# Kernel tuning notes

Hardware: AMD Instinct MI355X
Metric: run time of the kernel (lower is better)

The kernel has to match this reference:

```python
import jax, jax.numpy as jnp
import numpy as np

# dims: batch N, channels C, fine nodes V, coarse nodes VC, super nodes S, time L
N, C, V, VC, S, L, CO = 16, 32, 2048, 256, 64, 12, 32
N1, N2, N3, N4 = 0.8, 0.2, 0.2, 0.2  # residual fusion scales


def asym_adj(a):
    # D^-1 A row-normalization (sp.diags(d_inv) @ A), inf -> 0
    rowsum = jnp.sum(a, axis=1)
    d_inv = jnp.where(rowsum > 0, 1.0 / rowsum, 0.0)
    return a * d_inv[:, None]


def nconv(x, a):
    return jnp.einsum('ncvl,vw->ncwl', x, a)


def gcn(x, supports, W, b):
    h = jnp.concatenate([x, nconv(x, supports[0]), nconv(x, supports[1])], axis=1)
    return jnp.einsum('nkvl,ok->novl', h, W) + b[None, :, None, None]


def hgcn_forward(x, support, support_c, acs, afc, W, b):
    hf = gcn(x, support, W, b)                               # fine level  [N,CO,V,L]
    xc = jnp.einsum('vw,ncvl->ncwl', afc, x)                 # afc.T @ x   [N,C,VC,L]
    hc = gcn(xc, support_c, W, b)                            # coarse level [N,CO,VC,L]
    sxg = jnp.einsum('ws,ncwl->ncsl', acs, xc)               # acs.T @ afc.T @ x [N,C,S,L]
    # faithful reproduction of torch permute/reshape (mismatched flatten orders)
    hs_flat = jnp.transpose(sxg, (2, 1, 0, 3)).reshape(S, -1)  # [S, C*N*L]
    hst = jnp.transpose(sxg, (3, 0, 1, 2)).reshape(-1, S)      # [L*N*C, S]
    as_mat = jax.lax.stop_gradient(jax.nn.relu(hs_flat @ hst - 0.5))  # detached [S,S]
    sup_s = [jax.nn.softmax(asym_adj(as_mat), axis=-1),
             jax.nn.softmax(asym_adj(as_mat.T), axis=-1)]
    hs = gcn(sxg, sup_s, W, b)                               # super level [N,CO,S,L]
    # hierarchical relu-scaled residual fusions
    hc = hc + N1 * jax.nn.relu(jnp.einsum('ws,ncsl->ncwl', acs, hs))
    hf = hf + N2 * jax.nn.relu(jnp.einsum('vw,ncwl->ncvl', afc, hc))
    hc = hc + N3 * jax.nn.relu(jnp.einsum('vw,ncvl->ncwl', afc, hf))
    hs = hs + N4 * jax.nn.relu(jnp.einsum('ws,ncwl->ncsl', acs, hc))
    return hf, hc, hs


def setup_inputs() -> dict:
    key = jax.random.key(0)
    k = jax.random.split(key, 7)
    x = jax.random.normal(k[0], (N, C, V, L), jnp.float32)
    support = jax.nn.softmax(jax.random.normal(k[1], (2, V, V), jnp.float32), axis=-1)
    support_c = jax.nn.softmax(jax.random.normal(k[2], (2, VC, VC), jnp.float32), axis=-1)
    acs = jax.random.normal(k[3], (VC, S), jnp.float32) * 0.05
    afc = jax.random.normal(k[4], (V, VC), jnp.float32) * 0.02
    W = jax.random.normal(k[5], (CO, 3 * C), jnp.float32) * 0.05  # 1x1 conv weight
    b = jax.random.normal(k[6], (CO,), jnp.float32) * 0.01
    return {"x": x, "support": support, "support_c": support_c, "acs": acs,
            "afc": afc, "W": W, "b": b}


def reference(x, support, support_c, acs, afc, W, b):
    return hgcn_forward(x, support, support_c, acs, afc, W, b)
```

## Files before the change

kernel.cpp:

```cpp
#include <hip/hip_runtime.h>

constexpr int NB = 16;
constexpr int CC = 32;
constexpr int VV = 2048;
constexpr int VCC = 256;
constexpr int SS = 64;
constexpr int LL = 12;
constexpr int CO = 32;
constexpr long MM = (long)NB * CO * LL;

typedef __attribute__((ext_vector_type(8))) __bf16 bf16x8;
typedef __attribute__((ext_vector_type(4))) float f32x4;

__device__ __forceinline__ unsigned short f2bf(float f) {
    unsigned u = __float_as_uint(f);
    unsigned r = u + 0x7FFFu + ((u >> 16) & 1u);
    return (unsigned short)(r >> 16);
}

__device__ __forceinline__ void gl_lds16(const void* g, void* l) {
    __builtin_amdgcn_global_load_lds(
        (const __attribute__((address_space(1))) void*)g,
        (__attribute__((address_space(3))) void*)l, 16, 0, 0);
}

__global__ __launch_bounds__(256)
void transpose_vl(const float* __restrict__ in, float* __restrict__ out,
                  unsigned short* __restrict__ outb) {
    __shared__ float t[128 * 12];
    const long nc = blockIdx.y;
    const int v0 = blockIdx.x * 128;
    const float* src = in + (nc * VV + v0) * 12;
    for (int f = threadIdx.x; f < 128 * 12; f += 256) t[f] = src[f];
    __syncthreads();
    float* dst = out + nc * 12L * VV;
    unsigned short* dstb = outb + nc * 12L * VV;
    for (int g = threadIdx.x; g < 128 * 12; g += 256) {
        int l = g >> 7, vv = g & 127;
        const float v = t[vv * 12 + l];
        dst[(long)l * VV + v0 + vv] = v;
        dstb[(long)l * VV + v0 + vv] = f2bf(v);
    }
}

__global__ __launch_bounds__(256)
void transpose_lv(const float* __restrict__ in, float* __restrict__ out, int Kn, int TW) {
    __shared__ float t[128 * 12];
    const long nc = blockIdx.y;
    const int v0 = blockIdx.x * TW;
    const float* src = in + nc * 12L * Kn;
    for (int g = threadIdx.x; g < TW * 12; g += 256) {
        int l = g / TW, vv = g - l * TW;
        t[vv * 12 + l] = src[(long)l * Kn + v0 + vv];
    }
    __syncthreads();
    float* dst = out + (nc * Kn + v0) * 12L;
    for (int f = threadIdx.x; f < TW * 12; f += 256) dst[f] = t[f];
}

__global__ __launch_bounds__(256)
void transpose2d(const float* __restrict__ in, float* __restrict__ out, int rows, int cols) {
    __shared__ float t[32][33];
    const int r0 = blockIdx.y * 32, c0 = blockIdx.x * 32;
    const int ty = threadIdx.x / 32, tx = threadIdx.x % 32;
    for (int i = ty; i < 32; i += 8) t[i][tx] = in[(long)(r0 + i) * cols + c0 + tx];
    __syncthreads();
    for (int i = ty; i < 32; i += 8) out[(long)(c0 + i) * rows + r0 + tx] = t[tx][i];
}

__global__ __launch_bounds__(256)
void cvt_bf16_k(const float* __restrict__ in, unsigned short* __restrict__ out, long n) {
    long i = ((long)blockIdx.x * 256 + threadIdx.x) * 4;
    if (i >= n) return;
    const float4 v = *(const float4*)(in + i);
    ushort4 o;
    o.x = f2bf(v.x); o.y = f2bf(v.y); o.z = f2bf(v.z); o.w = f2bf(v.w);
    *(ushort4*)(out + i) = o;
}

__global__ __launch_bounds__(256)
void cvt_T_bf16_k(const float* __restrict__ in, unsigned short* __restrict__ out,
                  int R, int Ccols) {
    __shared__ float t[32][33];
    const int r0 = blockIdx.y * 32, c0 = blockIdx.x * 32;
    const int ty = threadIdx.x / 32, tx = threadIdx.x % 32;
    for (int i = ty; i < 32; i += 8) t[i][tx] = in[(long)(r0 + i) * Ccols + c0 + tx];
    __syncthreads();
    for (int i = ty; i < 32; i += 8) out[(long)(c0 + i) * R + r0 + tx] = f2bf(t[tx][i]);
}

__global__ __launch_bounds__(256)
void chanmix_fine(const float* __restrict__ in, const float* __restrict__ Wt,
                  float* __restrict__ y0, unsigned short* __restrict__ y12) {
    __shared__ float Ws[CO * 96];
    for (int idx = threadIdx.x; idx < CO * 96; idx += 256) Ws[idx] = Wt[idx];
    __syncthreads();
    const int nb = blockIdx.y;
    const int r = blockIdx.x * 256 + threadIdx.x;
    const int R = LL * VV;
    const int l = r / VV, k = r - l * VV;
    float xv[CC];
#pragma unroll
    for (int c = 0; c < CC; ++c) xv[c] = in[((long)(nb * CC + c)) * R + r];
    for (int o = 0; o < CO; ++o) {
        float a0 = 0.f, a1 = 0.f, a2 = 0.f;
#pragma unroll
        for (int c = 0; c < CC; ++c) {
            const float x = xv[c];
            a0 = fmaf(Ws[o * 96 + c], x, a0);
            a1 = fmaf(Ws[o * 96 + 32 + c], x, a1);
            a2 = fmaf(Ws[o * 96 + 64 + c], x, a2);
        }
        const long mrow = (long)(nb * CO + o) * LL + l;
        y0[mrow * VV + k] = a0;
        y12[mrow * 4096 + k] = f2bf(a1);
        y12[mrow * 4096 + 2048 + k] = f2bf(a2);
    }
}

__global__ __launch_bounds__(256)
void chanmix_k(const float* __restrict__ in, const float* __restrict__ Wt,
               int R, int Kn, float* __restrict__ o0,
               float* __restrict__ o1, int ld1) {
    __shared__ float Ws[CO * 96];
    for (int idx = threadIdx.x; idx < CO * 96; idx += 256) Ws[idx] = Wt[idx];
    __syncthreads();
    const int nb = blockIdx.y;
    const int r = blockIdx.x * 256 + threadIdx.x;
    if (r >= R) return;
    const int l = r / Kn, k = r - l * Kn;
    float xv[CC];
#pragma unroll
    for (int c = 0; c < CC; ++c) xv[c] = in[((long)(nb * CC + c)) * R + r];
    for (int o = 0; o < CO; ++o) {
        float a0 = 0.f, a1 = 0.f, a2 = 0.f;
#pragma unroll
        for (int c = 0; c < CC; ++c) {
            const float x = xv[c];
            a0 = fmaf(Ws[o * 96 + c], x, a0);
            a1 = fmaf(Ws[o * 96 + 32 + c], x, a1);
            a2 = fmaf(Ws[o * 96 + 64 + c], x, a2);
        }
        const long mrow = (long)(nb * CO + o) * LL + l;
        o0[mrow * Kn + k] = a0;
        o1[mrow * ld1 + k] = a1;
        o1[mrow * ld1 + Kn + k] = a2;
    }
}

template <bool RELU, bool ADDC0, bool BIAS>
__global__ __launch_bounds__(256)
void gemm_mfma(const unsigned short* __restrict__ A, int lda,
               const unsigned short* __restrict__ Bt, int ldb,
               const float* __restrict__ C0, int ldc,
               const float* __restrict__ bias,
               float* __restrict__ Out, int ldo, int K, float alpha) {
    __shared__ __align__(16) unsigned short As[128 * 64];
    __shared__ __align__(16) unsigned short Bs[128 * 64];
    const int tid = threadIdx.x;
    const int lane = tid & 63;
    const int w = tid >> 6;
    const long m0 = (long)blockIdx.y * 128;
    const int n0 = blockIdx.x * 128;

    long offA[4], offB[4];
#pragma unroll
    for (int q = 0; q < 4; ++q) {
        const int t = q * 256 + tid;
        const int row = t >> 3, pos = t & 7;
        const int lc = pos ^ (row & 7);
        offA[q] = (m0 + row) * (long)lda + lc * 8;
        offB[q] = (long)(n0 + row) * ldb + lc * 8;
    }
    const int wm = (w & 1) * 64, wn = (w >> 1) * 64;
    const int mrow = lane & 15;
    const int quad = lane >> 4;

    f32x4 acc[4][4];
#pragma unroll
    for (int i = 0; i < 4; ++i)
#pragma unroll
        for (int j = 0; j < 4; ++j) acc[i][j] = (f32x4){0.f, 0.f, 0.f, 0.f};

    for (int k0 = 0; k0 < K; k0 += 64) {
#pragma unroll
        for (int q = 0; q < 4; ++q)
            gl_lds16(A + offA[q] + k0, &As[(q * 256 + w * 64) * 8]);
#pragma unroll
        for (int q = 0; q < 4; ++q)
            gl_lds16(Bt + offB[q] + k0, &Bs[(q * 256 + w * 64) * 8]);
        __syncthreads();
#pragma unroll
        for (int ks = 0; ks < 2; ++ks) {
            bf16x8 af[4], bfr[4];
            const int pos = (ks * 4 + quad) ^ (mrow & 7);
#pragma unroll
            for (int tm = 0; tm < 4; ++tm) {
                const int r = wm + tm * 16 + mrow;
                af[tm] = *(const bf16x8*)&As[r * 64 + pos * 8];
            }
#pragma unroll
            for (int tn = 0; tn < 4; ++tn) {
                const int r = wn + tn * 16 + mrow;
                bfr[tn] = *(const bf16x8*)&Bs[r * 64 + pos * 8];
            }
#pragma unroll
            for (int tm = 0; tm < 4; ++tm)
#pragma unroll
                for (int tn = 0; tn < 4; ++tn)
                    acc[tm][tn] = __builtin_amdgcn_mfma_f32_16x16x32_bf16(
                        af[tm], bfr[tn], acc[tm][tn], 0, 0, 0);
        }
        __syncthreads();
    }

#pragma unroll
    for (int tm = 0; tm < 4; ++tm) {
#pragma unroll
        for (int tn = 0; tn < 4; ++tn) {
            const int n = n0 + wn + tn * 16 + mrow;
#pragma unroll
            for (int reg = 0; reg < 4; ++reg) {
                const long m = m0 + wm + tm * 16 + quad * 4 + reg;
                float p = acc[tm][tn][reg];
                if (RELU) p = fmaxf(p, 0.f);
                p *= alpha;
                float c = 0.f;
                if constexpr (ADDC0) c = C0[m * (long)ldc + n];
                if (BIAS) c += bias[(int)((m / LL) & (CO - 1))];
                Out[m * (long)ldo + n] = c + p;
            }
        }
    }
}

template <int BM, int BN, int BK, int TM, int TN, bool RELU, bool ADDC0, bool BIAS>
__global__ __launch_bounds__(256)
void gemm_k(const float* __restrict__ X, int ldx,
            const float* __restrict__ Bm, int ldb,
            const float* __restrict__ C0, int ldc,
            const float* __restrict__ bias,
            float* __restrict__ Out, int ldo, int K, float alpha) {
    constexpr int TX = BN / TN;
    constexpr int LX = (BM * BK) / 256;
    constexpr int LB = (BN * BK) / 256;
    __shared__ float Xs[BK][BM + 4];
    __shared__ float Bs[BK][BN + 4];
    const int tid = threadIdx.x;
    const int tx = tid % TX, ty = tid / TX;
    const long m0 = (long)blockIdx.y * BM;
    const int n0 = blockIdx.x * BN;
    const int xr = tid / (BK / LX);
    const int xcc = (tid % (BK / LX)) * LX;
    const int br = tid / (BN / LB);
    const int bc = (tid % (BN / LB)) * LB;

    float acc[TM][TN];
#pragma unroll
    for (int i = 0; i < TM; ++i)
#pragma unroll
        for (int j = 0; j < TN; ++j) acc[i][j] = 0.f;

    const float* Xp = X + (m0 + xr) * (long)ldx + xcc;
    const float* Bp = Bm + (long)br * ldb + n0 + bc;

    for (int k0 = 0; k0 < K; k0 += BK) {
        if constexpr (LX == 4) {
            const float4 v = *(const float4*)Xp;
            Xs[xcc + 0][xr] = v.x; Xs[xcc + 1][xr] = v.y;
            Xs[xcc + 2][xr] = v.z; Xs[xcc + 3][xr] = v.w;
        } else {
            const float2 v = *(const float2*)Xp;
            Xs[xcc + 0][xr] = v.x; Xs[xcc + 1][xr] = v.y;
        }
        if constexpr (LB == 4) {
            *(float4*)&Bs[br][bc] = *(const float4*)Bp;
        } else {
            *(float2*)&Bs[br][bc] = *(const float2*)Bp;
        }
        __syncthreads();
#pragma unroll
        for (int kk = 0; kk < BK; ++kk) {
            float a[TM], b[TN];
#pragma unroll
            for (int i = 0; i < TM; ++i) a[i] = Xs[kk][ty * TM + i];
#pragma unroll
            for (int j = 0; j < TN; ++j) b[j] = Bs[kk][tx * TN + j];
#pragma unroll
            for (int i = 0; i < TM; ++i)
#pragma unroll
                for (int j = 0; j < TN; ++j) acc[i][j] = fmaf(a[i], b[j], acc[i][j]);
        }
        __syncthreads();
        Xp += BK;
        Bp += (long)BK * ldb;
    }

#pragma unroll
    for (int i = 0; i < TM; ++i) {
        const long m = m0 + (long)ty * TM + i;
        float bv = 0.f;
        if (BIAS) bv = bias[(int)((m / LL) & (CO - 1))];
        const long obase = m * (long)ldo + n0 + tx * TN;
        long cbase = 0;
        if constexpr (ADDC0) cbase = m * (long)ldc + n0 + tx * TN;
#pragma unroll
        for (int j = 0; j < TN; ++j) {
            float p = acc[i][j];
            if (RELU) p = fmaxf(p, 0.f);
            p *= alpha;
            float c = 0.f;
            if constexpr (ADDC0) c = C0[cbase + j];
            Out[obase + j] = c + p + bv;
        }
    }
}

__global__ __launch_bounds__(256)
void zero_k(float* __restrict__ p, int n) {
    for (int i = blockIdx.x * 256 + threadIdx.x; i < n; i += gridDim.x * 256) p[i] = 0.f;
}

__global__ __launch_bounds__(256)
void asmat_split(const float* __restrict__ sxg, float* __restrict__ am_raw) {
    __shared__ float Us[128][65];
    __shared__ float Wsh[128][65];
    __shared__ int rA[128], rB[128];
    const int i0 = blockIdx.x * 128;
    const int tid = threadIdx.x;
    if (tid < 128) {
        const int i = i0 + tid;
        const int c = i / 192;
        const int rem = i - c * 192;
        const int n = rem / 12;
        const int l = rem - n * 12;
        rA[tid] = (n * 32 + c) * 12 + l;
        const int l2 = i >> 9;
        const int rem2 = i & 511;
        rB[tid] = ((rem2 >> 5) * 32 + (rem2 & 31)) * 12 + l2;
    }
    __syncthreads();
    for (int idx = tid; idx < 128 * 64; idx += 256) {
        const int r = idx >> 6, s = idx & 63;
        Us[r][s] = sxg[rA[r] * 64 + s];
        Wsh[r][s] = sxg[rB[r] * 64 + s];
    }
    __syncthreads();
    const int ts = (tid & 15) * 4;
    const int tt = (tid >> 4) * 4;
    float acc[4][4];
#pragma unroll
    for (int i2 = 0; i2 < 4; ++i2)
#pragma unroll
        for (int j = 0; j < 4; ++j) acc[i2][j] = 0.f;
    for (int k = 0; k < 128; ++k) {
        float a[4], bv[4];
#pragma unroll
        for (int i2 = 0; i2 < 4; ++i2) a[i2] = Us[k][ts + i2];
#pragma unroll
        for (int j = 0; j < 4; ++j) bv[j] = Wsh[k][tt + j];
#pragma unroll
        for (int i2 = 0; i2 < 4; ++i2)
#pragma unroll
            for (int j = 0; j < 4; ++j) acc[i2][j] = fmaf(a[i2], bv[j], acc[i2][j]);
    }
#pragma unroll
    for (int i2 = 0; i2 < 4; ++i2)
#pragma unroll
        for (int j = 0; j < 4; ++j)
            atomicAdd(&am_raw[(ts + i2) * 64 + tt + j], acc[i2][j]);
}

__global__ __launch_bounds__(64)
void supbuild_k(const float* __restrict__ am_raw, float* __restrict__ sup) {
    __shared__ float a[64][65];
    for (int idx = threadIdx.x; idx < 4096; idx += 64) {
        const float v = am_raw[idx] - 0.5f;
        a[idx >> 6][idx & 63] = v > 0.f ? v : 0.f;
    }
    __syncthreads();
    const int r = threadIdx.x;
    {
        float rs = 0.f;
        for (int j = 0; j < 64; ++j) rs += a[r][j];
        const float dinv = rs > 0.f ? 1.f / rs : 0.f;
        float mx = -1e30f;
        for (int j = 0; j < 64; ++j) mx = fmaxf(mx, a[r][j] * dinv);
        float se = 0.f;
        for (int j = 0; j < 64; ++j) se += expf(a[r][j] * dinv - mx);
        const float inv = 1.f / se;
        for (int j = 0; j < 64; ++j) sup[r * 64 + j] = expf(a[r][j] * dinv - mx) * inv;
    }
    {
        float rs = 0.f;
        for (int j = 0; j < 64; ++j) rs += a[j][r];
        const float dinv = rs > 0.f ? 1.f / rs : 0.f;
        float mx = -1e30f;
        for (int j = 0; j < 64; ++j) mx = fmaxf(mx, a[j][r] * dinv);
        float se = 0.f;
        for (int j = 0; j < 64; ++j) se += expf(a[j][r] * dinv - mx);
        const float inv = 1.f / se;
        for (int j = 0; j < 64; ++j) sup[4096 + r * 64 + j] = expf(a[j][r] * dinv - mx) * inv;
    }
}

extern "C" void kernel_launch(void* const* d_in, const int* in_sizes, int n_in,
                              void* d_out, int out_size, void* d_ws, size_t ws_size,
                              hipStream_t stream) {
    (void)in_sizes; (void)n_in; (void)out_size; (void)ws_size;
    const float* x    = (const float*)d_in[0];
    const float* sup  = (const float*)d_in[1];
    const float* supc = (const float*)d_in[2];
    const float* acs  = (const float*)d_in[3];
    const float* afc  = (const float*)d_in[4];
    const float* W    = (const float*)d_in[5];
    const float* b    = (const float*)d_in[6];
    float* ws = (float*)d_ws;

    float* xt = ws;
    unsigned short* Btu  = (unsigned short*)ws;
    unsigned short* afcb = (unsigned short*)(ws + 4194304);
    float* yc0  = ws + 4456448;
    float* yc12 = ws + 6029312;
    float* ys0  = ws + 9175040;
    float* ys12 = ws + 9568256;
    float* hc   = ws + 10354688;
    float* hs   = ws + 11927552;
    float* am   = ws + 12320768;
    float* sups = ws + 12324864;
    float* acsT = ws + 12333056;
    float* hf   = ws + 12582912;
    float* xc   = ws + 25165824;
    float* sxg  = ws + 26738688;
    unsigned short* afcTb = (unsigned short*)(ws + 27131904);

    float* out_f = (float*)d_out;
    unsigned short* xtb  = (unsigned short*)d_out;
    unsigned short* y12u = (unsigned short*)d_out;
    unsigned short* hfb  = (unsigned short*)d_out;
    unsigned short* hcb  = ((unsigned short*)d_out) + 12582912;
    float* hf_out = out_f;
    float* hc_out = out_f + 12582912;
    float* hs_out = out_f + 14155776;

    transpose_vl<<<dim3(VV / 128, NB * CC), 256, 0, stream>>>(x, xt, xtb);
    cvt_T_bf16_k<<<dim3(VCC / 32, VV / 32), 256, 0, stream>>>(afc, afcTb, VV, VCC);
    gemm_mfma<false, false, false><<<dim3(VCC / 128, MM / 128), 256, 0, stream>>>(
        xtb, VV, afcTb, VV, nullptr, 0, nullptr, xc, VCC, VV, 1.0f);
    chanmix_fine<<<dim3(96, 16), 256, 0, stream>>>(xt, W, hf, y12u);
    cvt_T_bf16_k<<<dim3(VV / 32, 2 * VV / 32), 256, 0, stream>>>(sup, Btu, 2 * VV, VV);
    cvt_bf16_k<<<dim3(512), 256, 0, stream>>>(afc, afcb, (long)VV * VCC);
    gemm_k<64, 64, 16, 4, 4, false, false, false><<<dim3(1, MM / 64), 256, 0, stream>>>(
        xc, VCC, acs, SS, nullptr, 0, nullptr, sxg, SS, VCC, 1.0f);
    chanmix_k<<<dim3(12, 16), 256, 0, stream>>>(xc, W, LL * VCC, VCC, yc0, yc12, 2 * VCC);
    chanmix_k<<<dim3(3, 16), 256, 0, stream>>>(sxg, W, LL * SS, SS, ys0, ys12, 2 * SS);
    zero_k<<<dim3(4), 256, 0, stream>>>(am, 4096);
    asmat_split<<<dim3(48), 256, 0, stream>>>(sxg, am);
    supbuild_k<<<dim3(1), 64, 0, stream>>>(am, sups);
    gemm_mfma<false, true, true><<<dim3(VV / 128, MM / 128), 256, 0, stream>>>(
        y12u, 4096, Btu, 4096, hf, VV, b, hf, VV, 4096, 1.0f);
    gemm_k<64, 64, 16, 4, 4, false, true, true><<<dim3(VCC / 64, MM / 64), 256, 0, stream>>>(
        yc12, 2 * VCC, supc, VCC, yc0, VCC, b, hc, VCC, 2 * VCC, 1.0f);
    gemm_k<64, 64, 16, 4, 4, false, true, true><<<dim3(1, MM / 64), 256, 0, stream>>>(
        ys12, 2 * SS, sups, SS, ys0, SS, b, hs, SS, 2 * SS, 1.0f);
    transpose2d<<<dim3(SS / 32, VCC / 32), 256, 0, stream>>>(acs, acsT, VCC, SS);
    gemm_k<64, 64, 16, 4, 4, true, true, false><<<dim3(VCC / 64, MM / 64), 256, 0, stream>>>(
        hs, SS, acsT, VCC, hc, VCC, nullptr, hc, VCC, SS, 0.8f);
    cvt_bf16_k<<<dim3(1536), 256, 0, stream>>>(hc, hcb, (long)MM * VCC);
    gemm_mfma<true, true, false><<<dim3(VV / 128, MM / 128), 256, 0, stream>>>(
        hcb, VCC, afcb, VCC, hf, VV, nullptr, hf, VV, VCC, 0.2f);
    cvt_bf16_k<<<dim3(12288), 256, 0, stream>>>(hf, hfb, (long)MM * VV);
    gemm_mfma<true, true, false><<<dim3(VCC / 128, MM / 128), 256, 0, stream>>>(
        hfb, VV, afcTb, VV, hc, VCC, nullptr, hc, VCC, VV, 0.2f);
    gemm_k<64, 64, 16, 4, 4, true, true, false><<<dim3(1, MM / 64), 256, 0, stream>>>(
        hc, VCC, acs, SS, hs, SS, nullptr, hs, SS, VCC, 0.2f);
    transpose_lv<<<dim3(VV / 128, NB * CO), 256, 0, stream>>>(hf, hf_out, VV, 128);
    transpose_lv<<<dim3(VCC / 128, NB * CO), 256, 0, stream>>>(hc, hc_out, VCC, 128);
    transpose_lv<<<dim3(1, NB * CO), 256, 0, stream>>>(hs, hs_out, SS, 64);
}
```

Before: 681.8 us.

## Fuse bf16 conversions into GEMM epilogues, narrow tiles for coarse GEMMs, swizzle grid

Removes the standalone float-to-bf16 conversion kernels for hc and hf by having the preceding GEMMs also write a bf16 copy in their epilogue. It also merges the two afc conversions (plain and transposed) into a single kernel. The mfma GEMM gains a template tile width so the GEMMs with N=256 use 64-wide tiles, which doubles their block count and fills more CUs. The wide GEMMs get a grouped block-index swizzle for better L2 reuse. The cost is extra bf16 stores in the epilogues, more template variants, and a moved afcb workspace slot.

```diff
diff --git a/kernel.cpp b/kernel.cpp
--- a/kernel.cpp
+++ b/kernel.cpp
@@ -69,16 +69,6 @@
 }
 
 __global__ __launch_bounds__(256)
-void cvt_bf16_k(const float* __restrict__ in, unsigned short* __restrict__ out, long n) {
-    long i = ((long)blockIdx.x * 256 + threadIdx.x) * 4;
-    if (i >= n) return;
-    const float4 v = *(const float4*)(in + i);
-    ushort4 o;
-    o.x = f2bf(v.x); o.y = f2bf(v.y); o.z = f2bf(v.z); o.w = f2bf(v.w);
-    *(ushort4*)(out + i) = o;
-}
-
-__global__ __launch_bounds__(256)
 void cvt_T_bf16_k(const float* __restrict__ in, unsigned short* __restrict__ out,
                   int R, int Ccols) {
     __shared__ float t[32][33];
@@ -90,6 +80,22 @@
 }
 
 __global__ __launch_bounds__(256)
+void cvt_afc_both(const float* __restrict__ in, unsigned short* __restrict__ outn,
+                  unsigned short* __restrict__ outt) {
+    __shared__ float t[32][33];
+    const int r0 = blockIdx.y * 32, c0 = blockIdx.x * 32;
+    const int ty = threadIdx.x / 32, tx = threadIdx.x % 32;
+    for (int i = ty; i < 32; i += 8) {
+        const float v = in[(long)(r0 + i) * VCC + c0 + tx];
+        t[i][tx] = v;
+        outn[(long)(r0 + i) * VCC + c0 + tx] = f2bf(v);
+    }
+    __syncthreads();
+    for (int i = ty; i < 32; i += 8) out_store:
+        outt[(long)(c0 + i) * VV + r0 + tx] = f2bf(t[tx][i]);
+}
+
+__global__ __launch_bounds__(256)
 void chanmix_fine(const float* __restrict__ in, const float* __restrict__ Wt,
                   float* __restrict__ y0, unsigned short* __restrict__ y12) {
     __shared__ float Ws[CO * 96];
@@ -148,51 +154,73 @@
     }
 }
 
-template <bool RELU, bool ADDC0, bool BIAS>
+template <int BN, bool SWIZ, bool RELU, bool ADDC0, bool BIAS, bool STB16>
 __global__ __launch_bounds__(256)
 void gemm_mfma(const unsigned short* __restrict__ A, int lda,
                const unsigned short* __restrict__ Bt, int ldb,
                const float* __restrict__ C0, int ldc,
                const float* __restrict__ bias,
-               float* __restrict__ Out, int ldo, int K, float alpha) {
+               float* __restrict__ Out, int ldo,
+               unsigned short* __restrict__ OutB, int K, float alpha) {
+    constexpr int TNT = BN / 32;
+    constexpr int QB = BN / 32;
+    constexpr int WN = BN / 2;
     __shared__ __align__(16) unsigned short As[128 * 64];
-    __shared__ __align__(16) unsigned short Bs[128 * 64];
+    __shared__ __align__(16) unsigned short Bs[BN * 64];
     const int tid = threadIdx.x;
     const int lane = tid & 63;
     const int w = tid >> 6;
-    const long m0 = (long)blockIdx.y * 128;
-    const int n0 = blockIdx.x * 128;
-
-    long offA[4], offB[4];
+
+    int pid_m, pid_n;
+    if constexpr (SWIZ) {
+        const int id = blockIdx.y * gridDim.x + blockIdx.x;
+        const int npg = 8 * gridDim.x;
+        const int rem = id % npg;
+        pid_m = (id / npg) * 8 + (rem & 7);
+        pid_n = rem >> 3;
+    } else {
+        pid_m = blockIdx.y;
+        pid_n = blockIdx.x;
+    }
+    const long m0 = (long)pid_m * 128;
+    const int n0 = pid_n * BN;
+
+    long offA[4], offB[QB];
 #pragma unroll
     for (int q = 0; q < 4; ++q) {
         const int t = q * 256 + tid;
         const int row = t >> 3, pos = t & 7;
         const int lc = pos ^ (row & 7);
         offA[q] = (m0 + row) * (long)lda + lc * 8;
+    }
+#pragma unroll
+    for (int q = 0; q < QB; ++q) {
+        const int t = q * 256 + tid;
+        const int row = t >> 3, pos = t & 7;
+        const int lc = pos ^ (row & 7);
         offB[q] = (long)(n0 + row) * ldb + lc * 8;
     }
-    const int wm = (w & 1) * 64, wn = (w >> 1) * 64;
+    const int wm = (w & 1) * 64, wn = (w >> 1) * WN;
     const int mrow = lane & 15;
     const int quad = lane >> 4;
 
-    f32x4 acc[4][4];
+    f32x4 acc[4][TNT];
 #pragma unroll
     for (int i = 0; i < 4; ++i)
 #pragma unroll
-        for (int j = 0; j < 4; ++j) acc[i][j] = (f32x4){0.f, 0.f, 0.f, 0.f};
+        for (int j = 0; j < TNT; ++j) acc[i][j] = (f32x4){0.f, 0.f, 0.f, 0.f};
 
     for (int k0 = 0; k0 < K; k0 += 64) {
 #pragma unroll
         for (int q = 0; q < 4; ++q)
             gl_lds16(A + offA[q] + k0, &As[(q * 256 + w * 64) * 8]);
 #pragma unroll
-        for (int q = 0; q < 4; ++q)
+        for (int q = 0; q < QB; ++q)
             gl_lds16(Bt + offB[q] + k0, &Bs[(q * 256 + w * 64) * 8]);
         __syncthreads();
 #pragma unroll
         for (int ks = 0; ks < 2; ++ks) {
-            bf16x8 af[4], bfr[4];
+            bf16x8 af[4], bfr[TNT];
             const int pos = (ks * 4 + quad) ^ (mrow & 7);
 #pragma unroll
             for (int tm = 0; tm < 4; ++tm) {
@@ -200,14 +228,14 @@
                 af[tm] = *(const bf16x8*)&As[r * 64 + pos * 8];
             }
 #pragma unroll
-            for (int tn = 0; tn < 4; ++tn) {
+            for (int tn = 0; tn < TNT; ++tn) {
                 const int r = wn + tn * 16 + mrow;
                 bfr[tn] = *(const bf16x8*)&Bs[r * 64 + pos * 8];
             }
 #pragma unroll
             for (int tm = 0; tm < 4; ++tm)
 #pragma unroll
-                for (int tn = 0; tn < 4; ++tn)
+                for (int tn = 0; tn < TNT; ++tn)
                     acc[tm][tn] = __builtin_amdgcn_mfma_f32_16x16x32_bf16(
                         af[tm], bfr[tn], acc[tm][tn], 0, 0, 0);
         }
@@ -217,7 +245,7 @@
 #pragma unroll
     for (int tm = 0; tm < 4; ++tm) {
 #pragma unroll
-        for (int tn = 0; tn < 4; ++tn) {
+        for (int tn = 0; tn < TNT; ++tn) {
             const int n = n0 + wn + tn * 16 + mrow;
 #pragma unroll
             for (int reg = 0; reg < 4; ++reg) {
@@ -228,19 +256,22 @@
                 float c = 0.f;
                 if constexpr (ADDC0) c = C0[m * (long)ldc + n];
                 if (BIAS) c += bias[(int)((m / LL) & (CO - 1))];
-                Out[m * (long)ldo + n] = c + p;
+                const float res = c + p;
+                Out[m * (long)ldo + n] = res;
+                if constexpr (STB16) OutB[m * (long)ldo + n] = f2bf(res);
             }
         }
     }
 }
 
-template <int BM, int BN, int BK, int TM, int TN, bool RELU, bool ADDC0, bool BIAS>
+template <int BM, int BN, int BK, int TM, int TN, bool RELU, bool ADDC0, bool BIAS, bool STB16>
 __global__ __launch_bounds__(256)
 void gemm_k(const float* __restrict__ X, int ldx,
             const float* __restrict__ Bm, int ldb,
             const float* __restrict__ C0, int ldc,
             const float* __restrict__ bias,
-            float* __restrict__ Out, int ldo, int K, float alpha) {
+            float* __restrict__ Out, int ldo,
+            unsigned short* __restrict__ outb, int K, float alpha) {
     constexpr int TX = BN / TN;
     constexpr int LX = (BM * BK) / 256;
     constexpr int LB = (BN * BK) / 256;
@@ -311,7 +342,9 @@
             p *= alpha;
             float c = 0.f;
             if constexpr (ADDC0) c = C0[cbase + j];
-            Out[obase + j] = c + p + bv;
+            const float res = c + p + bv;
+            Out[obase + j] = res;
+            if constexpr (STB16) outb[obase + j] = f2bf(res);
         }
     }
 }
@@ -418,8 +451,7 @@
     float* ws = (float*)d_ws;
 
     float* xt = ws;
-    unsigned short* Btu  = (unsigned short*)ws;
-    unsigned short* afcb = (unsigned short*)(ws + 4194304);
+    unsigned short* Btu = (unsigned short*)ws;
     float* yc0  = ws + 4456448;
     float* yc12 = ws + 6029312;
     float* ys0  = ws + 9175040;
@@ -433,6 +465,7 @@
     float* xc   = ws + 25165824;
     float* sxg  = ws + 26738688;
     unsigned short* afcTb = (unsigned short*)(ws + 27131904);
+    unsigned short* afcb  = (unsigned short*)(ws + 27394048);
 
     float* out_f = (float*)d_out;
     unsigned short* xtb  = (unsigned short*)d_out;
@@ -444,36 +477,33 @@
     float* hs_out = out_f + 14155776;
 
     transpose_vl<<<dim3(VV / 128, NB * CC), 256, 0, stream>>>(x, xt, xtb);
-    cvt_T_bf16_k<<<dim3(VCC / 32, VV / 32), 256, 0, stream>>>(afc, afcTb, VV, VCC);
-    gemm_mfma<false, false, false><<<dim3(VCC / 128, MM / 128), 256, 0, stream>>>(
-        xtb, VV, afcTb, VV, nullptr, 0, nullptr, xc, VCC, VV, 1.0f);
+    cvt_afc_both<<<dim3(VCC / 32, VV / 32), 256, 0, stream>>>(afc, afcb, afcTb);
+    gemm_mfma<64, false, false, false, false, false><<<dim3(VCC / 64, MM / 128), 256, 0, stream>>>(
+        xtb, VV, afcTb, VV, nullptr, 0, nullptr, xc, VCC, nullptr, VV, 1.0f);
     chanmix_fine<<<dim3(96, 16), 256, 0, stream>>>(xt, W, hf, y12u);
     cvt_T_bf16_k<<<dim3(VV / 32, 2 * VV / 32), 256, 0, stream>>>(sup, Btu, 2 * VV, VV);
-    cvt_bf16_k<<<dim3(512), 256, 0, stream>>>(afc, afcb, (long)VV * VCC);
-    gemm_k<64, 64, 16, 4, 4, false, false, false><<<dim3(1, MM / 64), 256, 0, stream>>>(
-        xc, VCC, acs, SS, nullptr, 0, nullptr, sxg, SS, VCC, 1.0f);
+    gemm_k<64, 64, 16, 4, 4, false, false, false, false><<<dim3(1, MM / 64), 256, 0, stream>>>(
+        xc, VCC, acs, SS, nullptr, 0, nullptr, sxg, SS, nullptr, VCC, 1.0f);
     chanmix_k<<<dim3(12, 16), 256, 0, stream>>>(xc, W, LL * VCC, VCC, yc0, yc12, 2 * VCC);
     chanmix_k<<<dim3(3, 16), 256, 0, stream>>>(sxg, W, LL * SS, SS, ys0, ys12, 2 * SS);
     zero_k<<<dim3(4), 256, 0, stream>>>(am, 4096);
     asmat_split<<<dim3(48), 256, 0, stream>>>(sxg, am);
     supbuild_k<<<dim3(1), 64, 0, stream>>>(am, sups);
-    gemm_mfma<false, true, true><<<dim3(VV / 128, MM / 128), 256, 0, stream>>>(
-        y12u, 4096, Btu, 4096, hf, VV, b, hf, VV, 4096, 1.0f);
-    gemm_k<64, 64, 16, 4, 4, false, true, true><<<dim3(VCC / 64, MM / 64), 256, 0, stream>>>(
-        yc12, 2 * VCC, supc, VCC, yc0, VCC, b, hc, VCC, 2 * VCC, 1.0f);
-    gemm_k<64, 64, 16, 4, 4, false, true, true><<<dim3(1, MM / 64), 256, 0, stream>>>(
-        ys12, 2 * SS, sups, SS, ys0, SS, b, hs, SS, 2 * SS, 1.0f);
+    gemm_mfma<128, true, false, true, true, false><<<dim3(VV / 128, MM / 128), 256, 0, stream>>>(
+        y12u, 4096, Btu, 4096, hf, VV, b, hf, VV, nullptr, 4096, 1.0f);
+    gemm_k<64, 64, 16, 4, 4, false, true, true, false><<<dim3(VCC / 64, MM / 64), 256, 0, stream>>>(
+        yc12, 2 * VCC, supc, VCC, yc0, VCC, b, hc, VCC, nullptr, 2 * VCC, 1.0f);
+    gemm_k<64, 64, 16, 4, 4, false, true, true, false><<<dim3(1, MM / 64), 256, 0, stream>>>(
+        ys12, 2 * SS, sups, SS, ys0, SS, b, hs, SS, nullptr, 2 * SS, 1.0f);
     transpose2d<<<dim3(SS / 32, VCC / 32), 256, 0, stream>>>(acs, acsT, VCC, SS);
-    gemm_k<64, 64, 16, 4, 4, true, true, false><<<dim3(VCC / 64, MM / 64), 256, 0, stream>>>(
-        hs, SS, acsT, VCC, hc, VCC, nullptr, hc, VCC, SS, 0.8f);
-    cvt_bf16_k<<<dim3(1536), 256, 0, stream>>>(hc, hcb, (long)MM * VCC);
-    gemm_mfma<true, true, false><<<dim3(VV / 128, MM / 128), 256, 0, stream>>>(
-        hcb, VCC, afcb, VCC, hf, VV, nullptr, hf, VV, VCC, 0.2f);
-    cvt_bf16_k<<<dim3(12288), 256, 0, stream>>>(hf, hfb, (long)MM * VV);
-    gemm_mfma<true, true, false><<<dim3(VCC / 128, MM / 128), 256, 0, stream>>>(
-        hfb, VV, afcTb, VV, hc, VCC, nullptr, hc, VCC, VV, 0.2f);
-    gemm_k<64, 64, 16, 4, 4, true, true, false><<<dim3(1, MM / 64), 256, 0, stream>>>(
-        hc, VCC, acs, SS, hs, SS, nullptr, hs, SS, VCC, 0.2f);
+    gemm_k<64, 64, 16, 4, 4, true, true, false, true><<<dim3(VCC / 64, MM / 64), 256, 0, stream>>>(
+        hs, SS, acsT, VCC, hc, VCC, nullptr, hc, VCC, hcb, SS, 0.8f);
+    gemm_mfma<128, true, true, true, false, true><<<dim3(VV / 128, MM / 128), 256, 0, stream>>>(
+        hcb, VCC, afcb, VCC, hf, VV, nullptr, hf, VV, hfb, VCC, 0.2f);
+    gemm_mfma<64, false, true, true, false, false><<<dim3(VCC / 64, MM / 128), 256, 0, stream>>>(
+        hfb, VV, afcTb, VV, hc, VCC, nullptr, hc, VCC, nullptr, VV, 0.2f);
+    gemm_k<64, 64, 16, 4, 4, true, true, false, false><<<dim3(1, MM / 64), 256, 0, stream>>>(
+        hc, VCC, acs, SS, hs, SS, nullptr, hs, SS, nullptr, VCC, 0.2f);
     transpose_lv<<<dim3(VV / 128, NB * CO), 256, 0, stream>>>(hf, hf_out, VV, 128);
     transpose_lv<<<dim3(VCC / 128, NB * CO), 256, 0, stream>>>(hc, hc_out, VCC, 128);
     transpose_lv<<<dim3(1, NB * CO), 256, 0, stream>>>(hs, hs_out, SS, 64);
```

New measurement: 645.9 us. 5.3% less time.
